# Kernel tuning notes

Measured on AMD Instinct MI355X. Metric: run time of the kernel, lower is better.

## Reference

```python
import jax, jax.numpy as jnp
import numpy as np

N = 100000
E = 1000000
IN_DIM = 64
ATT_DIM = 32


def setup_inputs() -> dict:
    key = jax.random.key(0)
    ks = jax.random.split(key, 9)
    x = jax.random.normal(ks[0], (N, IN_DIM), dtype=jnp.float32)
    src1 = jax.random.randint(ks[1], (E,), 0, N, dtype=jnp.int32)
    dst1 = jax.random.randint(ks[2], (E,), 0, N, dtype=jnp.int32)
    src2 = jax.random.randint(ks[3], (E,), 0, N, dtype=jnp.int32)
    dst2 = jax.random.randint(ks[4], (E,), 0, N, dtype=jnp.int32)
    # Learned params: w_o (in_dim -> att_dim), att (att_dim -> 1)
    W_o = jax.random.normal(ks[5], (IN_DIM, ATT_DIM), dtype=jnp.float32) / np.sqrt(IN_DIM)
    b_o = jnp.zeros((ATT_DIM,), dtype=jnp.float32)
    W_att = jax.random.normal(ks[6], (ATT_DIM, 1), dtype=jnp.float32) / np.sqrt(ATT_DIM)
    b_att = jnp.zeros((1,), dtype=jnp.float32)
    return {"x": x, "W_o": W_o, "b_o": b_o, "W_att": W_att, "b_att": b_att,
            "src1": src1, "dst1": dst1, "src2": src2, "dst2": dst2}


def _edge_softmax_agg(h, a, src, dst):
    """edge_softmax of source logits grouped by dst, then weighted sum of src feats."""
    a_e = a[src]  # [E] per-edge logit copied from source node (copy_u)
    m = jax.ops.segment_max(a_e, dst, num_segments=N)  # per-dst max for stability
    m = jnp.where(jnp.isfinite(m), m, 0.0)
    e = jnp.exp(a_e - jax.lax.stop_gradient(m)[dst])
    s = jax.ops.segment_sum(e, dst, num_segments=N)  # per-dst normalizer
    w = e / s[dst]  # normalized edge attention [E]
    # u_mul_e + sum reduction
    return jax.ops.segment_sum(h[src] * w[:, None], dst, num_segments=N)  # [N, in_dim]


def reference(x, W_o, b_o, W_att, b_att, src1, dst1, src2, dst2):
    # a = att(w_o(h))  (note: self.activation is defined but unused in forward)
    a = ((x @ W_o + b_o) @ W_att + b_att)[:, 0]  # [N]
    h1 = _edge_softmax_agg(x, a, src1, dst1)
    h2 = _edge_softmax_agg(x, a, src2, dst2)
    # multi_update_all cross-type 'mean' over the 2 edge types
    return (h1 + h2) * 0.5
```

## Files before the change

### kernel.cpp

```cpp
#include <hip/hip_runtime.h>
#include <hip/hip_bf16.h>

#define IN_DIM 64
#define BSHIFT 7
#define BSIZE  128
#define CHUNK  8192
#define MAXNB1 1024
#define CAPMAX 1600
#define GBLK   256

__device__ __forceinline__ float bflo(unsigned int u) { return __uint_as_float(u << 16); }
__device__ __forceinline__ float bfhi(unsigned int u) { return __uint_as_float(u & 0xFFFF0000u); }
__device__ __forceinline__ unsigned short f2bf(float f) {
    __hip_bfloat16 b = __float2bfloat16(f);
    return *reinterpret_cast<unsigned short*>(&b);
}

__global__ void logits_partition_kernel(const float* __restrict__ x,
                                        const float* __restrict__ W_o,
                                        const float* __restrict__ b_o,
                                        const float* __restrict__ W_att,
                                        const float* __restrict__ b_att,
                                        float* __restrict__ ea,
                                        unsigned short* __restrict__ xh, int N,
                                        const int* __restrict__ src1,
                                        const int* __restrict__ dst1,
                                        const int* __restrict__ src2,
                                        const int* __restrict__ dst2,
                                        int* __restrict__ gCtr,
                                        int* __restrict__ packed,
                                        int E, int NB1, int CAP, int chunks1) {
    __shared__ int hist[MAXNB1];
    __shared__ int base[MAXNB1];
    __shared__ float vsh[IN_DIM];
    __shared__ float csh;
    int pb = 2 * chunks1;
    if (blockIdx.x < pb) {
        int b = blockIdx.x;
        int type = (b >= chunks1) ? 1 : 0;
        int ci = type ? (b - chunks1) : b;
        const int* src = type ? src2 : src1;
        const int* dst = type ? dst2 : dst1;
        int e0 = ci * CHUNK;
        int e1 = min(E, e0 + CHUNK);
        for (int i = threadIdx.x; i < NB1; i += blockDim.x) hist[i] = 0;
        __syncthreads();
        for (int e = e0 + threadIdx.x; e < e1; e += blockDim.x)
            atomicAdd(&hist[dst[e] >> BSHIFT], 1);
        __syncthreads();
        for (int i = threadIdx.x; i < NB1; i += blockDim.x) {
            int h = hist[i];
            base[i] = h ? atomicAdd(&gCtr[type * NB1 + i], h) : 0;
            hist[i] = 0;
        }
        __syncthreads();
        for (int e = e0 + threadIdx.x; e < e1; e += blockDim.x) {
            int d = dst[e];
            int bk = d >> BSHIFT;
            int rank = base[bk] + atomicAdd(&hist[bk], 1);
            if (rank < CAP)
                packed[(size_t)(type * NB1 + bk) * CAP + rank] =
                    src[e] | ((d & (BSIZE - 1)) << 17);
        }
    } else {
        int t = threadIdx.x;
        if (t < IN_DIM) {
            float acc = 0.f;
#pragma unroll
            for (int k = 0; k < 32; ++k) acc += W_o[t * 32 + k] * W_att[k];
            vsh[t] = acc;
        }
        if (t == IN_DIM) {
            float acc = b_att[0];
#pragma unroll
            for (int k = 0; k < 32; ++k) acc += b_o[k] * W_att[k];
            csh = acc;
        }
        __syncthreads();
        int node = (blockIdx.x - pb) * 16 + (t >> 4);
        int fq = t & 15;
        if (node >= N) return;
        const float4 xv = *(const float4*)(x + (size_t)node * 64 + fq * 4);
        ushort4 st;
        st.x = f2bf(xv.x); st.y = f2bf(xv.y); st.z = f2bf(xv.z); st.w = f2bf(xv.w);
        *(ushort4*)(xh + (size_t)node * 64 + fq * 4) = st;
        float val = xv.x * vsh[fq * 4 + 0] + xv.y * vsh[fq * 4 + 1] +
                    xv.z * vsh[fq * 4 + 2] + xv.w * vsh[fq * 4 + 3];
        val += __shfl_xor(val, 1);
        val += __shfl_xor(val, 2);
        val += __shfl_xor(val, 4);
        val += __shfl_xor(val, 8);
        if (fq == 0) ea[node] = expf(val + csh);
    }
}

__global__ __launch_bounds__(GBLK, 5) void csr_gather_kernel(
        const int* __restrict__ gCtr,
        const int* __restrict__ packed,
        const float* __restrict__ ea,
        const unsigned short* __restrict__ xh,
        float* __restrict__ out, int N, int NB1, int CAP) {
    __shared__ int2 pae[2][CAPMAX];
    __shared__ int  hist[2][BSIZE];
    __shared__ int  exv [2][BSIZE];
    __shared__ int  cur [BSIZE];
    int nb = blockIdx.x;
    int t = threadIdx.x;

#pragma unroll
    for (int type = 0; type < 2; ++type) {
        int r = type * NB1 + nb;
        int cnt = min(gCtr[r], CAP);
        const int* seg = packed + (size_t)r * CAP;
        for (int i = t; i < cnt; i += GBLK) pae[type][i].x = seg[i];
        if (t < BSIZE) hist[type][t] = 0;
        __syncthreads();
        for (int i = t; i < cnt; i += GBLK)
            atomicAdd(&hist[type][pae[type][i].x >> 17], 1);
        __syncthreads();
        int v = 0, val = 0;
        if (t < BSIZE) { v = hist[type][t]; val = v; cur[t] = v; }
        __syncthreads();
        for (int off = 1; off < BSIZE; off <<= 1) {
            int u = 0;
            if (t < BSIZE && t >= off) u = cur[t - off];
            __syncthreads();
            if (t < BSIZE) { val += u; cur[t] = val; }
            __syncthreads();
        }
        if (t < BSIZE) { exv[type][t] = val - v; cur[t] = val - v; }
        __syncthreads();
        for (int i = t; i < cnt; i += GBLK) {
            int p = pae[type][i].x;
            int pos = atomicAdd(&cur[p >> 17], 1);
            pae[type][pos].y = p & 0x1FFFF;
        }
        __syncthreads();
        for (int i = t; i < cnt; i += GBLK) {
            int s2 = pae[type][i].y;
            pae[type][i].x = s2;
            pae[type][i].y = __float_as_int(ea[s2]);
        }
        __syncthreads();
    }

    int gid = t >> 3;
    int fl  = t & 7;

    for (int ni = 0; ni < 4; ++ni) {
        int dl = (ni << 5) + gid;
        float rr[8] = {0,0,0,0,0,0,0,0};
#pragma unroll
        for (int type = 0; type < 2; ++type) {
            int k0 = exv[type][dl];
            int deg = hist[type][dl];
            if (deg <= 0) continue;
            float accP[8] = {0,0,0,0,0,0,0,0};
            float accQ[8] = {0,0,0,0,0,0,0,0};
            float ewP = 0.f, ewQ = 0.f;
            int h = deg >> 1;
            for (int j = 0; j < h; ++j) {
                int2 p1 = pae[type][k0 + j];
                int2 p2 = pae[type][k0 + h + j];
                const uint4 v1 = *(const uint4*)(xh + (size_t)p1.x * 64 + (fl << 3));
                const uint4 v2 = *(const uint4*)(xh + (size_t)p2.x * 64 + (fl << 3));
                float e1 = __int_as_float(p1.y);
                float e2 = __int_as_float(p2.y);
                ewP += e1; ewQ += e2;
                accP[0] = fmaf(e1, bflo(v1.x), accP[0]);
                accP[1] = fmaf(e1, bfhi(v1.x), accP[1]);
                accP[2] = fmaf(e1, bflo(v1.y), accP[2]);
                accP[3] = fmaf(e1, bfhi(v1.y), accP[3]);
                accP[4] = fmaf(e1, bflo(v1.z), accP[4]);
                accP[5] = fmaf(e1, bfhi(v1.z), accP[5]);
                accP[6] = fmaf(e1, bflo(v1.w), accP[6]);
                accP[7] = fmaf(e1, bfhi(v1.w), accP[7]);
                accQ[0] = fmaf(e2, bflo(v2.x), accQ[0]);
                accQ[1] = fmaf(e2, bfhi(v2.x), accQ[1]);
                accQ[2] = fmaf(e2, bflo(v2.y), accQ[2]);
                accQ[3] = fmaf(e2, bfhi(v2.y), accQ[3]);
                accQ[4] = fmaf(e2, bflo(v2.z), accQ[4]);
                accQ[5] = fmaf(e2, bfhi(v2.z), accQ[5]);
                accQ[6] = fmaf(e2, bflo(v2.w), accQ[6]);
                accQ[7] = fmaf(e2, bfhi(v2.w), accQ[7]);
            }
            if (deg & 1) {
                int2 p1 = pae[type][k0 + deg - 1];
                const uint4 v1 = *(const uint4*)(xh + (size_t)p1.x * 64 + (fl << 3));
                float e1 = __int_as_float(p1.y);
                ewP += e1;
                accP[0] = fmaf(e1, bflo(v1.x), accP[0]);
                accP[1] = fmaf(e1, bfhi(v1.x), accP[1]);
                accP[2] = fmaf(e1, bflo(v1.y), accP[2]);
                accP[3] = fmaf(e1, bfhi(v1.y), accP[3]);
                accP[4] = fmaf(e1, bflo(v1.z), accP[4]);
                accP[5] = fmaf(e1, bfhi(v1.z), accP[5]);
                accP[6] = fmaf(e1, bflo(v1.w), accP[6]);
                accP[7] = fmaf(e1, bfhi(v1.w), accP[7]);
            }
            float inv = 1.f / (ewP + ewQ);
#pragma unroll
            for (int k = 0; k < 8; ++k)
                rr[k] = fmaf(accP[k] + accQ[k], inv, rr[k]);
        }
        int node = (nb << BSHIFT) + dl;
        if (node < N) {
            float* op = out + (size_t)node * 64 + (fl << 3);
            *(float4*)op       = make_float4(0.5f * rr[0], 0.5f * rr[1], 0.5f * rr[2], 0.5f * rr[3]);
            *(float4*)(op + 4) = make_float4(0.5f * rr[4], 0.5f * rr[5], 0.5f * rr[6], 0.5f * rr[7]);
        }
    }
}

extern "C" void kernel_launch(void* const* d_in, const int* in_sizes, int n_in,
                              void* d_out, int out_size, void* d_ws, size_t ws_size,
                              hipStream_t stream) {
    const float* x     = (const float*)d_in[0];
    const float* W_o   = (const float*)d_in[1];
    const float* b_o   = (const float*)d_in[2];
    const float* W_att = (const float*)d_in[3];
    const float* b_att = (const float*)d_in[4];
    const int*   src1  = (const int*)d_in[5];
    const int*   dst1  = (const int*)d_in[6];
    const int*   src2  = (const int*)d_in[7];
    const int*   dst2  = (const int*)d_in[8];
    float* out = (float*)d_out;

    const int N = in_sizes[0] / IN_DIM;
    const int E = in_sizes[5];
    const int NB1 = (N + BSIZE - 1) >> BSHIFT;
    const int avg = (E + NB1 - 1) / NB1;
    int CAP = avg + avg / 6 + 32;
    if (CAP > CAPMAX) CAP = CAPMAX;

    char* wp = (char*)d_ws;
    auto take = [&](size_t bytes) { char* p = wp; wp += (bytes + 63) & ~63ull; return p; };
    float* ea          = (float*)take((size_t)N * 4);
    int* gCtr          = (int*)take((size_t)2 * NB1 * 4);
    unsigned short* xh = (unsigned short*)take((size_t)N * 64 * 2);
    int* packed        = (int*)take((size_t)2 * NB1 * CAP * 4);

    hipMemsetAsync(gCtr, 0, (size_t)2 * NB1 * sizeof(int), stream);

    int chunks1 = (E + CHUNK - 1) / CHUNK;
    int logitBlocks = (N + 15) / 16;
    logits_partition_kernel<<<2 * chunks1 + logitBlocks, 256, 0, stream>>>(
        x, W_o, b_o, W_att, b_att, ea, xh, N,
        src1, dst1, src2, dst2, gCtr, packed, E, NB1, CAP, chunks1);

    csr_gather_kernel<<<NB1, GBLK, 0, stream>>>(gCtr, packed, ea, xh, out,
                                                N, NB1, CAP);
}
```

Before: 99.04 us.

## Stage partitioned edges in LDS sorted by bucket before coalesced global writes

The partition phase now computes a block-local exclusive scan of the bucket histogram and scatters packed edges into shared memory in bucket order. It then writes them out linearly, so consecutive threads store to contiguous ranges within each bucket rather than random global addresses. Block size rises to 512 threads, and logit blocks each cover 32 nodes. The cost is much more LDS per block (about 56KB), which limits occupancy, plus extra scan synchronisation.

```diff
diff --git a/kernel.cpp b/kernel.cpp
--- a/kernel.cpp
+++ b/kernel.cpp
@@ -5,6 +5,7 @@
 #define BSHIFT 7
 #define BSIZE  128
 #define CHUNK  8192
+#define PBLK   512
 #define MAXNB1 1024
 #define CAPMAX 1600
 #define GBLK   256
@@ -16,25 +17,31 @@
     return *reinterpret_cast<unsigned short*>(&b);
 }
 
-__global__ void logits_partition_kernel(const float* __restrict__ x,
-                                        const float* __restrict__ W_o,
-                                        const float* __restrict__ b_o,
-                                        const float* __restrict__ W_att,
-                                        const float* __restrict__ b_att,
-                                        float* __restrict__ ea,
-                                        unsigned short* __restrict__ xh, int N,
-                                        const int* __restrict__ src1,
-                                        const int* __restrict__ dst1,
-                                        const int* __restrict__ src2,
-                                        const int* __restrict__ dst2,
-                                        int* __restrict__ gCtr,
-                                        int* __restrict__ packed,
-                                        int E, int NB1, int CAP, int chunks1) {
+__global__ __launch_bounds__(PBLK) void logits_partition_kernel(
+        const float* __restrict__ x,
+        const float* __restrict__ W_o,
+        const float* __restrict__ b_o,
+        const float* __restrict__ W_att,
+        const float* __restrict__ b_att,
+        float* __restrict__ ea,
+        unsigned short* __restrict__ xh, int N,
+        const int* __restrict__ src1,
+        const int* __restrict__ dst1,
+        const int* __restrict__ src2,
+        const int* __restrict__ dst2,
+        int* __restrict__ gCtr,
+        int* __restrict__ packed,
+        int E, int NB1, int CAP, int chunks1) {
+    __shared__ int spk[CHUNK];
+    __shared__ unsigned short sbk[CHUNK];
     __shared__ int hist[MAXNB1];
-    __shared__ int base[MAXNB1];
+    __shared__ int lbase[MAXNB1];
+    __shared__ int gb2[MAXNB1];
+    __shared__ int scr[PBLK];
     __shared__ float vsh[IN_DIM];
     __shared__ float csh;
     int pb = 2 * chunks1;
+    int t = threadIdx.x;
     if (blockIdx.x < pb) {
         int b = blockIdx.x;
         int type = (b >= chunks1) ? 1 : 0;
@@ -43,27 +50,49 @@
         const int* dst = type ? dst2 : dst1;
         int e0 = ci * CHUNK;
         int e1 = min(E, e0 + CHUNK);
-        for (int i = threadIdx.x; i < NB1; i += blockDim.x) hist[i] = 0;
-        __syncthreads();
-        for (int e = e0 + threadIdx.x; e < e1; e += blockDim.x)
+        int cnt = e1 - e0;
+        for (int i = t; i < MAXNB1; i += PBLK) hist[i] = 0;
+        __syncthreads();
+        for (int e = e0 + t; e < e1; e += PBLK)
             atomicAdd(&hist[dst[e] >> BSHIFT], 1);
         __syncthreads();
-        for (int i = threadIdx.x; i < NB1; i += blockDim.x) {
+        int a0 = hist[2 * t], a1 = hist[2 * t + 1];
+        int s = a0 + a1;
+        scr[t] = s;
+        __syncthreads();
+        int val = s;
+        for (int off = 1; off < PBLK; off <<= 1) {
+            int u = (t >= off) ? scr[t - off] : 0;
+            __syncthreads();
+            val += u;
+            scr[t] = val;
+            __syncthreads();
+        }
+        int ex = val - s;
+        lbase[2 * t] = ex;
+        lbase[2 * t + 1] = ex + a0;
+        __syncthreads();
+        for (int i = t; i < NB1; i += PBLK) {
             int h = hist[i];
-            base[i] = h ? atomicAdd(&gCtr[type * NB1 + i], h) : 0;
-            hist[i] = 0;
-        }
-        __syncthreads();
-        for (int e = e0 + threadIdx.x; e < e1; e += blockDim.x) {
+            gb2[i] = (h ? atomicAdd(&gCtr[type * NB1 + i], h) : 0) - lbase[i];
+            hist[i] = lbase[i];
+        }
+        __syncthreads();
+        for (int e = e0 + t; e < e1; e += PBLK) {
             int d = dst[e];
             int bk = d >> BSHIFT;
-            int rank = base[bk] + atomicAdd(&hist[bk], 1);
-            if (rank < CAP)
-                packed[(size_t)(type * NB1 + bk) * CAP + rank] =
-                    src[e] | ((d & (BSIZE - 1)) << 17);
+            int lrank = atomicAdd(&hist[bk], 1);
+            spk[lrank] = src[e] | ((d & (BSIZE - 1)) << 17);
+            sbk[lrank] = (unsigned short)bk;
+        }
+        __syncthreads();
+        for (int i = t; i < cnt; i += PBLK) {
+            int bk = sbk[i];
+            int lrk = gb2[bk] + i;
+            if (lrk < CAP)
+                packed[(size_t)(type * NB1 + bk) * CAP + lrk] = spk[i];
         }
     } else {
-        int t = threadIdx.x;
         if (t < IN_DIM) {
             float acc = 0.f;
 #pragma unroll
@@ -77,7 +106,7 @@
             csh = acc;
         }
         __syncthreads();
-        int node = (blockIdx.x - pb) * 16 + (t >> 4);
+        int node = (blockIdx.x - pb) * 32 + (t >> 4);
         int fq = t & 15;
         if (node >= N) return;
         const float4 xv = *(const float4*)(x + (size_t)node * 64 + fq * 4);
@@ -243,8 +272,8 @@
     hipMemsetAsync(gCtr, 0, (size_t)2 * NB1 * sizeof(int), stream);
 
     int chunks1 = (E + CHUNK - 1) / CHUNK;
-    int logitBlocks = (N + 15) / 16;
-    logits_partition_kernel<<<2 * chunks1 + logitBlocks, 256, 0, stream>>>(
+    int logitBlocks = (N + 31) / 32;
+    logits_partition_kernel<<<2 * chunks1 + logitBlocks, PBLK, 0, stream>>>(
         x, W_o, b_o, W_att, b_att, ea, xh, N,
         src1, dst1, src2, dst2, gCtr, packed, E, NB1, CAP, chunks1);
 
```

Measured after the change: 81.19 us. -18.0%, faster.
